# Optimization experiments

Measured on AMD Instinct MI355X. Metric: run time of the kernel, lower is better.

Reference implementation:

```python
import jax, jax.numpy as jnp
import numpy as np
from jax import lax

START_IDX = 7
STOP_IDX = 8
TAGSET = 9
VOCAB = 50257
EMB = 512
HID = 1024  # bidirectional: HID//2 per direction
SEQ = 8192


def _lstm_dir(x, Wih, Whh, bih, bhh, reverse):
    # x: [T, EMB]; Wih: [4H, EMB]; Whh: [4H, H]
    H = Whh.shape[1]
    xproj = x @ Wih.T + bih  # big GEMM hoisted out of the scan: [T, 4H]

    def step(carry, xp):
        h, c = carry
        g = xp + h @ Whh.T + bhh
        i, f, gg, o = jnp.split(g, 4)
        i = jax.nn.sigmoid(i)
        f = jax.nn.sigmoid(f)
        gg = jnp.tanh(gg)
        o = jax.nn.sigmoid(o)
        c = f * c + i * gg
        h = o * jnp.tanh(c)
        return (h, c), h

    init = (jnp.zeros((H,), x.dtype), jnp.zeros((H,), x.dtype))
    _, hs = lax.scan(step, init, xproj, reverse=reverse)
    return hs  # [T, H]


def _viterbi(feats, transitions):
    # feats: [T, TAGSET]; transitions[next, prev]
    init = jnp.full((TAGSET,), -10000.0, feats.dtype).at[START_IDX].set(0.0)

    def step(fv, feat):
        scores = fv[None, :] + transitions       # [next, prev]
        bp = jnp.argmax(scores, axis=1)          # best prev per next tag
        fv_new = jnp.max(scores, axis=1) + feat
        return fv_new, bp

    fv, bptrs = lax.scan(step, init, feats)
    terminal = fv + transitions[STOP_IDX]
    best = jnp.argmax(terminal)
    path_score = terminal[best]

    def back(c, bp):
        return bp[c], c

    _, path = lax.scan(back, best, bptrs, reverse=True)  # path[t] = tag at t
    return path_score, path.astype(jnp.int32)


def setup_inputs() -> dict:
    key = jax.random.key(0)
    ks = jax.random.split(key, 13)
    H = HID // 2
    s = lambda *sh: 0.05
    inp = {
        'sentence': jax.random.randint(ks[0], (SEQ,), 0, VOCAB, dtype=jnp.int32),
        'emb': jax.random.normal(ks[1], (VOCAB + 100, EMB), jnp.float32) * 0.05,
        'Wih_f': jax.random.normal(ks[2], (4 * H, EMB), jnp.float32) * 0.05,
        'Whh_f': jax.random.normal(ks[3], (4 * H, H), jnp.float32) * 0.05,
        'bih_f': jnp.zeros((4 * H,), jnp.float32),
        'bhh_f': jnp.zeros((4 * H,), jnp.float32),
        'Wih_b': jax.random.normal(ks[4], (4 * H, EMB), jnp.float32) * 0.05,
        'Whh_b': jax.random.normal(ks[5], (4 * H, H), jnp.float32) * 0.05,
        'bih_b': jnp.zeros((4 * H,), jnp.float32),
        'bhh_b': jnp.zeros((4 * H,), jnp.float32),
        'W_out': jax.random.normal(ks[6], (TAGSET, HID), jnp.float32) * 0.05,
        'b_out': jnp.zeros((TAGSET,), jnp.float32),
    }
    trans = jax.random.normal(ks[7], (TAGSET, TAGSET), jnp.float32)
    trans = trans.at[START_IDX, :].set(-10000.0)
    trans = trans.at[:, STOP_IDX].set(-10000.0)
    inp['transitions'] = trans
    return inp


def reference(sentence, emb, Wih_f, Whh_f, bih_f, bhh_f, Wih_b, Whh_b, bih_b, bhh_b, W_out, b_out, transitions):
    x = emb[sentence]                                   # [T, EMB]
    h_f = _lstm_dir(x, Wih_f, Whh_f, bih_f, bhh_f, reverse=False)
    h_b = _lstm_dir(x, Wih_b, Whh_b, bih_b, bhh_b, reverse=True)
    lstm_out = jnp.concatenate([h_f, h_b], axis=-1)     # [T, HID]
    feats = lstm_out @ W_out.T + b_out                  # [T, TAGSET]
    score, path = _viterbi(feats, transitions)
    return score, path
```

## Files before the change

### kernel.cpp

```cpp
#include <hip/hip_runtime.h>
#include <hip/hip_bf16.h>


#define T_SEQ   8192
#define EMB     512
#define HDIM    512
#define G4      2048
#define NBLK    16
#define POISON  0x7F7F7F7Fu

__global__ __launch_bounds__(256) void gemm_xproj(
    const int* __restrict__ sentence, const float* __restrict__ emb,
    const float* __restrict__ Wih_f, const float* __restrict__ Wih_b,
    const float* __restrict__ bih_f, const float* __restrict__ bhh_f,
    const float* __restrict__ bih_b, const float* __restrict__ bhh_b,
    float* __restrict__ xprojb)
{
    __shared__ float As[16][68];
    __shared__ float Bs[16][68];
    __shared__ int   srow[64];

    const int tid = threadIdx.x;
    const int bm = blockIdx.x;
    const int bn = blockIdx.y;
    const int fwd = (bn < 32);
    const float* W = fwd ? Wih_f : Wih_b;
    const int jbase = fwd ? bn * 64 : bn * 64 - 2048;

    if (tid < 64) srow[tid] = sentence[bm * 64 + tid];
    __syncthreads();

    const int tx = tid & 15, ty = tid >> 4;
    const int lkk = tid & 15;
    const int lr  = tid >> 4;
    int sr[4];
    #pragma unroll
    for (int i = 0; i < 4; ++i) sr[i] = srow[lr + i * 16];

    float acc[4][4] = {};

    for (int kb = 0; kb < 32; ++kb) {
        const int k0 = kb * 16;
        #pragma unroll
        for (int i = 0; i < 4; ++i) {
            const int r = lr + i * 16;
            As[lkk][r] = emb[(size_t)sr[i] * EMB + k0 + lkk];
            Bs[lkk][r] = W[(size_t)(jbase + r) * EMB + k0 + lkk];
        }
        __syncthreads();
        #pragma unroll
        for (int kk = 0; kk < 16; ++kk) {
            const float4 a = *(const float4*)&As[kk][ty * 4];
            const float4 b = *(const float4*)&Bs[kk][tx * 4];
            acc[0][0] = fmaf(a.x, b.x, acc[0][0]); acc[0][1] = fmaf(a.x, b.y, acc[0][1]);
            acc[0][2] = fmaf(a.x, b.z, acc[0][2]); acc[0][3] = fmaf(a.x, b.w, acc[0][3]);
            acc[1][0] = fmaf(a.y, b.x, acc[1][0]); acc[1][1] = fmaf(a.y, b.y, acc[1][1]);
            acc[1][2] = fmaf(a.y, b.z, acc[1][2]); acc[1][3] = fmaf(a.y, b.w, acc[1][3]);
            acc[2][0] = fmaf(a.z, b.x, acc[2][0]); acc[2][1] = fmaf(a.z, b.y, acc[2][1]);
            acc[2][2] = fmaf(a.z, b.z, acc[2][2]); acc[2][3] = fmaf(a.z, b.w, acc[2][3]);
            acc[3][0] = fmaf(a.w, b.x, acc[3][0]); acc[3][1] = fmaf(a.w, b.y, acc[3][1]);
            acc[3][2] = fmaf(a.w, b.z, acc[3][2]); acc[3][3] = fmaf(a.w, b.w, acc[3][3]);
        }
        __syncthreads();
    }

    const float* b1 = fwd ? bih_f : bih_b;
    const float* b2 = fwd ? bhh_f : bhh_b;
    const int jj = jbase + tx * 4;
    const float4 bias = make_float4(b1[jj] + b2[jj], b1[jj + 1] + b2[jj + 1],
                                    b1[jj + 2] + b2[jj + 2], b1[jj + 3] + b2[jj + 3]);
    #pragma unroll
    for (int i = 0; i < 4; ++i) {
        const int t = bm * 64 + ty * 4 + i;
        float4 v = make_float4(acc[i][0] + bias.x, acc[i][1] + bias.y,
                               acc[i][2] + bias.z, acc[i][3] + bias.w);
        *(float4*)&xprojb[(size_t)t * 4096 + bn * 64 + tx * 4] = v;
    }
}

__device__ __forceinline__ float fsig(float x) { return 1.0f / (1.0f + __expf(-x)); }
__device__ __forceinline__ float ftanh(float x) {
    const float e = __expf(-2.0f * fabsf(x));
    return copysignf((1.0f - e) / (1.0f + e), x);
}

__global__ __launch_bounds__(256, 1) void lstm_scan(
    const float* __restrict__ xprojb,
    const float* __restrict__ Whh_f, const float* __restrict__ Whh_b,
    unsigned int* __restrict__ hseq)
{
    const int tid = threadIdx.x;
    const int blk = blockIdx.x;
    const int dir = blk & 1;
    const int sub = blk >> 1;
    const float* Whh = dir ? Whh_b : Whh_f;
    unsigned int* hs = hseq + (size_t)dir * T_SEQ * HDIM;

    const int q  = tid & 7;
    const int rg = tid >> 3;
    const int g  = rg >> 3;
    const int mbase = (rg & 7) * 4;

    float w[4][64];
    #pragma unroll
    for (int r = 0; r < 4; ++r) {
        const float* src = Whh + ((size_t)(g * 512 + sub * 32 + mbase + r) << 9) + (q << 6);
        #pragma unroll
        for (int i = 0; i < 16; ++i) {
            const float4 v = *(const float4*)(src + i * 4);
            w[r][i * 4 + 0] = v.x; w[r][i * 4 + 1] = v.y;
            w[r][i * 4 + 2] = v.z; w[r][i * 4 + 3] = v.w;
        }
    }

    __shared__ float hlds[8 * 68];
    __shared__ float gsum[128];
    float c_state = 0.0f;

    const int k0 = tid * 2;
    const int a0 = k0 + (k0 >> 6) * 4;

    #pragma unroll 1
    for (int s = 0; s < T_SEQ; ++s) {
        const int t = dir ? (T_SEQ - 1 - s) : s;

        float xp0 = 0.f, xp1 = 0.f, xp2 = 0.f, xp3 = 0.f;
        if (tid < 32) {
            const float* xr = xprojb + (size_t)t * 4096 + dir * 2048 + sub * 32 + tid;
            xp0 = xr[0]; xp1 = xr[512]; xp2 = xr[1024]; xp3 = xr[1536];
        }

        if (s == 0) {
            hlds[a0] = 0.0f; hlds[a0 + 1] = 0.0f;
        } else {
            const int tprev = dir ? (t + 1) : (t - 1);
            unsigned int* hp = hs + (size_t)tprev * HDIM + k0;
            unsigned int u0, u1;
            u0 = __hip_atomic_load(hp, __ATOMIC_RELAXED, __HIP_MEMORY_SCOPE_AGENT);
            while (u0 == POISON) {
                __builtin_amdgcn_s_sleep(1);
                u0 = __hip_atomic_load(hp, __ATOMIC_RELAXED, __HIP_MEMORY_SCOPE_AGENT);
            }
            u1 = __hip_atomic_load(hp + 1, __ATOMIC_RELAXED, __HIP_MEMORY_SCOPE_AGENT);
            while (u1 == POISON) {
                __builtin_amdgcn_s_sleep(1);
                u1 = __hip_atomic_load(hp + 1, __ATOMIC_RELAXED, __HIP_MEMORY_SCOPE_AGENT);
            }
            hlds[a0]     = __uint_as_float(u0);
            hlds[a0 + 1] = __uint_as_float(u1);
        }
        __syncthreads();

        float acc[4] = {0.f, 0.f, 0.f, 0.f};
        const float* hb = &hlds[q * 68];
        #pragma unroll
        for (int ii = 0; ii < 16; ++ii) {
            const float4 hv = *(const float4*)(hb + ii * 4);
            #pragma unroll
            for (int r = 0; r < 4; ++r) {
                acc[r] = fmaf(w[r][ii * 4 + 0], hv.x, acc[r]);
                acc[r] = fmaf(w[r][ii * 4 + 1], hv.y, acc[r]);
                acc[r] = fmaf(w[r][ii * 4 + 2], hv.z, acc[r]);
                acc[r] = fmaf(w[r][ii * 4 + 3], hv.w, acc[r]);
            }
        }
        #pragma unroll
        for (int d = 1; d <= 4; d <<= 1) {
            #pragma unroll
            for (int r = 0; r < 4; ++r) acc[r] += __shfl_xor(acc[r], d);
        }
        if (q == 0)
            *(float4*)&gsum[rg * 4] = make_float4(acc[0], acc[1], acc[2], acc[3]);
        __syncthreads();

        if (tid < 32) {
            const int m = tid;
            const float gi = gsum[m]      + xp0;
            const float gf = gsum[32 + m] + xp1;
            const float gg = gsum[64 + m] + xp2;
            const float go = gsum[96 + m] + xp3;
            const float i_ = fsig(gi);
            const float f_ = fsig(gf);
            const float g_ = ftanh(gg);
            const float o_ = fsig(go);
            c_state = fmaf(f_, c_state, i_ * g_);
            const float h = o_ * ftanh(c_state);
            __hip_atomic_store(hs + (size_t)t * HDIM + sub * 32 + m, __float_as_uint(h),
                               __ATOMIC_RELAXED, __HIP_MEMORY_SCOPE_AGENT);
        }
    }
}

__global__ __launch_bounds__(256) void feats_kernel(
    const float* __restrict__ hseq, const float* __restrict__ W_out,
    const float* __restrict__ b_out, float* __restrict__ feats)
{
    const int idx = blockIdx.x * 256 + threadIdx.x;
    if (idx >= T_SEQ * 9) return;
    const int t = idx / 9;
    const int n = idx - t * 9;
    const float4* hf = (const float4*)(hseq + (size_t)t * HDIM);
    const float4* hb = (const float4*)(hseq + (size_t)(T_SEQ + t) * HDIM);
    const float4* wf = (const float4*)(W_out + (size_t)n * 1024);
    const float4* wb = wf + 128;
    float acc = b_out[n];
    #pragma unroll 8
    for (int i = 0; i < 128; ++i) {
        const float4 a = hf[i], w = wf[i];
        acc = fmaf(a.x, w.x, acc); acc = fmaf(a.y, w.y, acc);
        acc = fmaf(a.z, w.z, acc); acc = fmaf(a.w, w.w, acc);
    }
    #pragma unroll 8
    for (int i = 0; i < 128; ++i) {
        const float4 a = hb[i], w = wb[i];
        acc = fmaf(a.x, w.x, acc); acc = fmaf(a.y, w.y, acc);
        acc = fmaf(a.z, w.z, acc); acc = fmaf(a.w, w.w, acc);
    }
    feats[idx] = acc;
}

__global__ __launch_bounds__(64) void viterbi_kernel(
    const float* __restrict__ feats, const float* __restrict__ trans,
    unsigned long long* __restrict__ bpw, float* __restrict__ out)
{
    const int lane = threadIdx.x;
    __shared__ __align__(16) float flds[1024 * 9];
    __shared__ unsigned char path_lds[T_SEQ];

    float tr[9];
    #pragma unroll
    for (int p = 0; p < 9; ++p) tr[p] = 0.f;
    float tstop = 0.f;
    if (lane < 9) {
        #pragma unroll
        for (int p = 0; p < 9; ++p) tr[p] = trans[lane * 9 + p];
        tstop = trans[8 * 9 + lane];
    }
    float fv = (lane == 7) ? 0.0f : -10000.0f;

    for (int ch = 0; ch < 8; ++ch) {
        const float4* src = (const float4*)(feats + (size_t)ch * 9216);
        #pragma unroll
        for (int i = 0; i < 36; ++i)
            ((float4*)flds)[lane + i * 64] = src[lane + i * 64];
        __syncthreads();

        for (int tt = 0; tt < 1024; ++tt) {
            const int t = ch * 1024 + tt;
            const float f0 = __shfl(fv, 0), f1 = __shfl(fv, 1), f2 = __shfl(fv, 2);
            const float f3 = __shfl(fv, 3), f4 = __shfl(fv, 4), f5 = __shfl(fv, 5);
            const float f6 = __shfl(fv, 6), f7 = __shfl(fv, 7), f8 = __shfl(fv, 8);
            const float s0 = f0 + tr[0], s1 = f1 + tr[1], s2 = f2 + tr[2];
            const float s3 = f3 + tr[3], s4 = f4 + tr[4], s5 = f5 + tr[5];
            const float s6 = f6 + tr[6], s7 = f7 + tr[7], s8 = f8 + tr[8];
            const float mx = fmaxf(fmaxf(fmaxf(fmaxf(s0, s1), fmaxf(s2, s3)),
                                         fmaxf(fmaxf(s4, s5), fmaxf(s6, s7))), s8);
            const unsigned bits =
                (s0 >= mx ? 1u : 0u)   | (s1 >= mx ? 2u : 0u)   | (s2 >= mx ? 4u : 0u) |
                (s3 >= mx ? 8u : 0u)   | (s4 >= mx ? 16u : 0u)  | (s5 >= mx ? 32u : 0u) |
                (s6 >= mx ? 64u : 0u)  | (s7 >= mx ? 128u : 0u) | (s8 >= mx ? 256u : 0u);
            const int bi = __ffs(bits) - 1;
            const float feat = (lane < 9) ? flds[tt * 9 + lane] : 0.0f;
            fv = mx + feat;
            const unsigned long long b0 = __ballot(bi & 1);
            const unsigned long long b1 = __ballot(bi & 2);
            const unsigned long long b2 = __ballot(bi & 4);
            const unsigned long long b3 = __ballot(bi & 8);
            if (lane == 0) {
                bpw[t] = (b0 & 511ull) | ((b1 & 511ull) << 9) |
                         ((b2 & 511ull) << 18) | ((b3 & 511ull) << 27);
            }
        }
        __syncthreads();
    }

    const float term = fv + tstop;
    const float t0 = __shfl(term, 0), t1 = __shfl(term, 1), t2 = __shfl(term, 2);
    const float t3 = __shfl(term, 3), t4 = __shfl(term, 4), t5 = __shfl(term, 5);
    const float t6 = __shfl(term, 6), t7 = __shfl(term, 7), t8 = __shfl(term, 8);
    const float mxt = fmaxf(fmaxf(fmaxf(fmaxf(t0, t1), fmaxf(t2, t3)),
                                  fmaxf(fmaxf(t4, t5), fmaxf(t6, t7))), t8);
    const unsigned bitst =
        (t0 >= mxt ? 1u : 0u)   | (t1 >= mxt ? 2u : 0u)   | (t2 >= mxt ? 4u : 0u) |
        (t3 >= mxt ? 8u : 0u)   | (t4 >= mxt ? 16u : 0u)  | (t5 >= mxt ? 32u : 0u) |
        (t6 >= mxt ? 64u : 0u)  | (t7 >= mxt ? 128u : 0u) | (t8 >= mxt ? 256u : 0u);
    const int best = __ffs(bitst) - 1;

    if (lane == 0) {
        out[0] = mxt;
        int c = best;
        path_lds[T_SEQ - 1] = (unsigned char)c;
        for (int thi = T_SEQ - 2; thi >= 15; thi -= 16) {
            const int tlo = thi - 15;
            unsigned long long wbuf[16];
            #pragma unroll
            for (int i = 0; i < 16; ++i) wbuf[i] = bpw[tlo + 1 + i];
            #pragma unroll
            for (int i = 15; i >= 0; --i) {
                const unsigned long long wv = wbuf[i];
                c = (int)((wv >> c) & 1ull) |
                    ((int)((wv >> (9 + c)) & 1ull) << 1) |
                    ((int)((wv >> (18 + c)) & 1ull) << 2) |
                    ((int)((wv >> (27 + c)) & 1ull) << 3);
                path_lds[tlo + i] = (unsigned char)c;
            }
        }
        for (int t2i = 14; t2i >= 0; --t2i) {
            const unsigned long long wv = bpw[t2i + 1];
            c = (int)((wv >> c) & 1ull) |
                ((int)((wv >> (9 + c)) & 1ull) << 1) |
                ((int)((wv >> (18 + c)) & 1ull) << 2) |
                ((int)((wv >> (27 + c)) & 1ull) << 3);
            path_lds[t2i] = (unsigned char)c;
        }
    }
    __syncthreads();
    #pragma unroll 4
    for (int i = 0; i < T_SEQ / 64; ++i) {
        const int t = i * 64 + lane;
        out[1 + t] = (float)path_lds[t];
    }
}

extern "C" void kernel_launch(void* const* d_in, const int* in_sizes, int n_in,
                              void* d_out, int out_size, void* d_ws, size_t ws_size,
                              hipStream_t stream)
{
    (void)in_sizes; (void)n_in; (void)out_size; (void)ws_size;

    const int*   sentence = (const int*)  d_in[0];
    const float* emb      = (const float*)d_in[1];
    const float* Wih_f    = (const float*)d_in[2];
    const float* Whh_f    = (const float*)d_in[3];
    const float* bih_f    = (const float*)d_in[4];
    const float* bhh_f    = (const float*)d_in[5];
    const float* Wih_b    = (const float*)d_in[6];
    const float* Whh_b    = (const float*)d_in[7];
    const float* bih_b    = (const float*)d_in[8];
    const float* bhh_b    = (const float*)d_in[9];
    const float* W_out    = (const float*)d_in[10];
    const float* b_out    = (const float*)d_in[11];
    const float* trans    = (const float*)d_in[12];

    float* ws      = (float*)d_ws;
    float* xprojb  = ws;
    float* hseq    = ws + (size_t)T_SEQ * 4096;
    float* feats   = hseq + (size_t)2 * T_SEQ * HDIM;
    unsigned long long* bpw = (unsigned long long*)(feats + (size_t)T_SEQ * 9);

    hipMemsetAsync(hseq, 0x7F, (size_t)2 * T_SEQ * HDIM * sizeof(float), stream);

    gemm_xproj<<<dim3(128, 64), 256, 0, stream>>>(
        sentence, emb, Wih_f, Wih_b, bih_f, bhh_f, bih_b, bhh_b, xprojb);

    lstm_scan<<<dim3(32), 256, 0, stream>>>(
        xprojb, Whh_f, Whh_b, (unsigned int*)hseq);

    feats_kernel<<<dim3((T_SEQ * 9 + 255) / 256), 256, 0, stream>>>(
        hseq, W_out, b_out, feats);

    viterbi_kernel<<<dim3(1), 64, 0, stream>>>(feats, trans, bpw, (float*)d_out);
}
```

Baseline: 20.12 ms.

## Restructure LSTM scan into warp-specialized blocks with counter-based sync and 64-bit h exchange

The recurrent scan now runs 64 blocks of 320 threads instead of 32 blocks of 256, so each block owns a 16-unit slice. Four matvec wavefronts each hold two Whh rows over a 128-wide k chunk in registers. A dedicated wavefront applies the gate nonlinearities, and the waves coordinate through a shared-memory counter and flag instead of __syncthreads. The block's own h slice is forwarded through LDS, and h values are published and polled as packed 64-bit words. The aim is to shorten the per-step critical path of barriers and global polling, at the cost of busy-wait spinning in shared memory and more blocks that must all be co-resident.

New measurement: 17.13 ms (median of 2 runs). -14.9%, faster.

```diff
diff --git a/kernel.cpp b/kernel.cpp
--- a/kernel.cpp
+++ b/kernel.cpp
@@ -5,9 +5,9 @@
 #define T_SEQ   8192
 #define EMB     512
 #define HDIM    512
-#define G4      2048
-#define NBLK    16
-#define POISON  0x7F7F7F7Fu
+#define NSUB    32
+#define SLICE   16
+#define POISON64 0x7F7F7F7F7F7F7F7Full
 
 __global__ __launch_bounds__(256) void gemm_xproj(
     const int* __restrict__ sentence, const float* __restrict__ emb,
@@ -83,110 +83,145 @@
     const float e = __expf(-2.0f * fabsf(x));
     return copysignf((1.0f - e) / (1.0f + e), x);
 }
-
-__global__ __launch_bounds__(256, 1) void lstm_scan(
+__device__ __forceinline__ unsigned long long pack2(float a, float b) {
+    return (unsigned long long)__float_as_uint(a) |
+           ((unsigned long long)__float_as_uint(b) << 32);
+}
+
+__global__ __launch_bounds__(320, 1) void lstm_scan(
     const float* __restrict__ xprojb,
     const float* __restrict__ Whh_f, const float* __restrict__ Whh_b,
-    unsigned int* __restrict__ hseq)
-{
-    const int tid = threadIdx.x;
-    const int blk = blockIdx.x;
-    const int dir = blk & 1;
-    const int sub = blk >> 1;
-    const float* Whh = dir ? Whh_b : Whh_f;
-    unsigned int* hs = hseq + (size_t)dir * T_SEQ * HDIM;
-
-    const int q  = tid & 7;
-    const int rg = tid >> 3;
-    const int g  = rg >> 3;
-    const int mbase = (rg & 7) * 4;
-
-    float w[4][64];
-    #pragma unroll
-    for (int r = 0; r < 4; ++r) {
-        const float* src = Whh + ((size_t)(g * 512 + sub * 32 + mbase + r) << 9) + (q << 6);
-        #pragma unroll
-        for (int i = 0; i < 16; ++i) {
-            const float4 v = *(const float4*)(src + i * 4);
-            w[r][i * 4 + 0] = v.x; w[r][i * 4 + 1] = v.y;
-            w[r][i * 4 + 2] = v.z; w[r][i * 4 + 3] = v.w;
-        }
-    }
-
-    __shared__ float hlds[8 * 68];
-    __shared__ float gsum[128];
-    float c_state = 0.0f;
-
-    const int k0 = tid * 2;
-    const int a0 = k0 + (k0 >> 6) * 4;
-
-    #pragma unroll 1
-    for (int s = 0; s < T_SEQ; ++s) {
-        const int t = dir ? (T_SEQ - 1 - s) : s;
-
-        float xp0 = 0.f, xp1 = 0.f, xp2 = 0.f, xp3 = 0.f;
-        if (tid < 32) {
-            const float* xr = xprojb + (size_t)t * 4096 + dir * 2048 + sub * 32 + tid;
-            xp0 = xr[0]; xp1 = xr[512]; xp2 = xr[1024]; xp3 = xr[1536];
-        }
-
-        if (s == 0) {
-            hlds[a0] = 0.0f; hlds[a0 + 1] = 0.0f;
-        } else {
-            const int tprev = dir ? (t + 1) : (t - 1);
-            unsigned int* hp = hs + (size_t)tprev * HDIM + k0;
-            unsigned int u0, u1;
-            u0 = __hip_atomic_load(hp, __ATOMIC_RELAXED, __HIP_MEMORY_SCOPE_AGENT);
-            while (u0 == POISON) {
-                __builtin_amdgcn_s_sleep(1);
-                u0 = __hip_atomic_load(hp, __ATOMIC_RELAXED, __HIP_MEMORY_SCOPE_AGENT);
-            }
-            u1 = __hip_atomic_load(hp + 1, __ATOMIC_RELAXED, __HIP_MEMORY_SCOPE_AGENT);
-            while (u1 == POISON) {
-                __builtin_amdgcn_s_sleep(1);
-                u1 = __hip_atomic_load(hp + 1, __ATOMIC_RELAXED, __HIP_MEMORY_SCOPE_AGENT);
-            }
-            hlds[a0]     = __uint_as_float(u0);
-            hlds[a0 + 1] = __uint_as_float(u1);
-        }
-        __syncthreads();
-
-        float acc[4] = {0.f, 0.f, 0.f, 0.f};
-        const float* hb = &hlds[q * 68];
-        #pragma unroll
-        for (int ii = 0; ii < 16; ++ii) {
-            const float4 hv = *(const float4*)(hb + ii * 4);
+    float* __restrict__ hseq)
+{
+    const int tid  = threadIdx.x;
+    const int lane = tid & 63;
+    const int wv   = tid >> 6;
+    const int blk  = blockIdx.x;
+    const int dir  = blk & 1;
+    const int sub  = blk >> 1;
+    const float* __restrict__ Whh = dir ? Whh_b : Whh_f;
+    float* hs = hseq + (size_t)dir * T_SEQ * HDIM;
+
+    __shared__ __align__(16) float hst[2][4][128];
+    __shared__ __align__(16) float partials[2][4][64];
+    __shared__ __align__(8)  float ownh[2][SLICE];
+    __shared__ unsigned int cnt;
+    __shared__ unsigned int ownflag;
+
+    if (tid == 0) { cnt = 0u; ownflag = 0u; }
+    __syncthreads();
+
+    if (wv == 0) {
+        float c_state = 0.0f;
+        const int  m   = lane & 15;
+        const bool fin = lane < 16;
+        #pragma unroll 1
+        for (int s = 0; s < T_SEQ; ++s) {
+            const int t = dir ? (T_SEQ - 1 - s) : s;
+            const int p = s & 1;
+            float xp0 = 0.f, xp1 = 0.f, xp2 = 0.f, xp3 = 0.f;
+            if (fin) {
+                const float* xr = xprojb + (size_t)t * 4096 + dir * 2048 + sub * SLICE + m;
+                xp0 = xr[0]; xp1 = xr[512]; xp2 = xr[1024]; xp3 = xr[1536];
+            }
+            const unsigned target = 4u * (unsigned)(s + 1);
+            while (__hip_atomic_load(&cnt, __ATOMIC_ACQUIRE,
+                                     __HIP_MEMORY_SCOPE_WORKGROUP) < target) {}
+            float h = 0.0f;
+            if (fin) {
+                const float si = partials[p][0][m]      + partials[p][1][m]
+                               + partials[p][2][m]      + partials[p][3][m];
+                const float sf = partials[p][0][16 + m] + partials[p][1][16 + m]
+                               + partials[p][2][16 + m] + partials[p][3][16 + m];
+                const float sg = partials[p][0][32 + m] + partials[p][1][32 + m]
+                               + partials[p][2][32 + m] + partials[p][3][32 + m];
+                const float so = partials[p][0][48 + m] + partials[p][1][48 + m]
+                               + partials[p][2][48 + m] + partials[p][3][48 + m];
+                const float i_ = fsig(si + xp0);
+                const float f_ = fsig(sf + xp1);
+                const float g_ = ftanh(sg + xp2);
+                const float o_ = fsig(so + xp3);
+                c_state = fmaf(f_, c_state, i_ * g_);
+                h = o_ * ftanh(c_state);
+                ownh[p][m] = h;
+            }
+            if (lane == 0)
+                __hip_atomic_store(&ownflag, (unsigned)(s + 1), __ATOMIC_RELEASE,
+                                   __HIP_MEMORY_SCOPE_WORKGROUP);
+            const float ha = __shfl(h, lane * 2);
+            const float hb = __shfl(h, lane * 2 + 1);
+            if (lane < 8) {
+                unsigned long long* hp =
+                    (unsigned long long*)(hs + (size_t)t * HDIM + sub * SLICE);
+                __hip_atomic_store(hp + lane, pack2(ha, hb), __ATOMIC_RELAXED,
+                                   __HIP_MEMORY_SCOPE_AGENT);
+            }
+        }
+    } else {
+        const int c  = wv - 1;
+        const int rp = lane & 31;
+        const int kh = lane >> 5;
+        const int r0 = rp * 2;
+        const int grow  = (r0 >> 4) * 512 + sub * SLICE + (r0 & 15);
+        const int kbase = c * 128 + kh * 64;
+        float w0[64], w1[64];
+        {
+            const float* src0 = Whh + (size_t)grow * 512 + kbase;
+            const float* src1 = src0 + 512;
             #pragma unroll
-            for (int r = 0; r < 4; ++r) {
-                acc[r] = fmaf(w[r][ii * 4 + 0], hv.x, acc[r]);
-                acc[r] = fmaf(w[r][ii * 4 + 1], hv.y, acc[r]);
-                acc[r] = fmaf(w[r][ii * 4 + 2], hv.z, acc[r]);
-                acc[r] = fmaf(w[r][ii * 4 + 3], hv.w, acc[r]);
-            }
-        }
-        #pragma unroll
-        for (int d = 1; d <= 4; d <<= 1) {
+            for (int j = 0; j < 16; ++j) {
+                const float4 a = *(const float4*)(src0 + 4 * j);
+                const float4 b = *(const float4*)(src1 + 4 * j);
+                w0[4*j] = a.x; w0[4*j+1] = a.y; w0[4*j+2] = a.z; w0[4*j+3] = a.w;
+                w1[4*j] = b.x; w1[4*j+1] = b.y; w1[4*j+2] = b.z; w1[4*j+3] = b.w;
+            }
+        }
+        const bool ownlane = (c == (sub >> 3)) && ((lane >> 3) == (sub & 7));
+
+        #pragma unroll 1
+        for (int s = 0; s < T_SEQ; ++s) {
+            const int t = dir ? (T_SEQ - 1 - s) : s;
+            const int p = s & 1;
+            float2 hv2;
+            if (s == 0) {
+                hv2 = make_float2(0.f, 0.f);
+            } else if (ownlane) {
+                while (__hip_atomic_load(&ownflag, __ATOMIC_ACQUIRE,
+                                         __HIP_MEMORY_SCOPE_WORKGROUP) < (unsigned)s) {}
+                const int pp = (s - 1) & 1;
+                const int j  = lane & 7;
+                hv2.x = ownh[pp][2 * j];
+                hv2.y = ownh[pp][2 * j + 1];
+            } else {
+                const int tprev = dir ? (t + 1) : (t - 1);
+                const unsigned long long* hp =
+                    (const unsigned long long*)(hs + (size_t)tprev * HDIM) + c * 64 + lane;
+                unsigned long long u = __hip_atomic_load(hp, __ATOMIC_RELAXED,
+                                                         __HIP_MEMORY_SCOPE_AGENT);
+                while (u == POISON64)
+                    u = __hip_atomic_load(hp, __ATOMIC_RELAXED, __HIP_MEMORY_SCOPE_AGENT);
+                hv2.x = __uint_as_float((unsigned)(u & 0xffffffffull));
+                hv2.y = __uint_as_float((unsigned)(u >> 32));
+            }
+            ((float2*)&hst[p][c][0])[lane] = hv2;
+
+            float acc0 = 0.f, acc1 = 0.f;
+            const float4* hb = (const float4*)&hst[p][c][kh * 64];
             #pragma unroll
-            for (int r = 0; r < 4; ++r) acc[r] += __shfl_xor(acc[r], d);
-        }
-        if (q == 0)
-            *(float4*)&gsum[rg * 4] = make_float4(acc[0], acc[1], acc[2], acc[3]);
-        __syncthreads();
-
-        if (tid < 32) {
-            const int m = tid;
-            const float gi = gsum[m]      + xp0;
-            const float gf = gsum[32 + m] + xp1;
-            const float gg = gsum[64 + m] + xp2;
-            const float go = gsum[96 + m] + xp3;
-            const float i_ = fsig(gi);
-            const float f_ = fsig(gf);
-            const float g_ = ftanh(gg);
-            const float o_ = fsig(go);
-            c_state = fmaf(f_, c_state, i_ * g_);
-            const float h = o_ * ftanh(c_state);
-            __hip_atomic_store(hs + (size_t)t * HDIM + sub * 32 + m, __float_as_uint(h),
-                               __ATOMIC_RELAXED, __HIP_MEMORY_SCOPE_AGENT);
+            for (int j = 0; j < 16; ++j) {
+                const float4 hv = hb[j];
+                acc0 = fmaf(w0[4*j],   hv.x, acc0); acc1 = fmaf(w1[4*j],   hv.x, acc1);
+                acc0 = fmaf(w0[4*j+1], hv.y, acc0); acc1 = fmaf(w1[4*j+1], hv.y, acc1);
+                acc0 = fmaf(w0[4*j+2], hv.z, acc0); acc1 = fmaf(w1[4*j+2], hv.z, acc1);
+                acc0 = fmaf(w0[4*j+3], hv.w, acc0); acc1 = fmaf(w1[4*j+3], hv.w, acc1);
+            }
+            acc0 += __shfl_xor(acc0, 32);
+            acc1 += __shfl_xor(acc1, 32);
+            if (lane < 32)
+                ((float2*)&partials[p][c][0])[lane] = make_float2(acc0, acc1);
+            if (lane == 0)
+                __hip_atomic_fetch_add(&cnt, 1u, __ATOMIC_RELEASE,
+                                       __HIP_MEMORY_SCOPE_WORKGROUP);
         }
     }
 }
@@ -353,8 +388,8 @@
     gemm_xproj<<<dim3(128, 64), 256, 0, stream>>>(
         sentence, emb, Wih_f, Wih_b, bih_f, bhh_f, bih_b, bhh_b, xprojb);
 
-    lstm_scan<<<dim3(32), 256, 0, stream>>>(
-        xprojb, Whh_f, Whh_b, (unsigned int*)hseq);
+    lstm_scan<<<dim3(64), 320, 0, stream>>>(
+        xprojb, Whh_f, Whh_b, hseq);
 
     feats_kernel<<<dim3((T_SEQ * 9 + 255) / 256), 256, 0, stream>>>(
         hseq, W_out, b_out, feats);
```
